# Performance work log

Measured on AMD Instinct MI355X. Metric: run time of the kernel, lower is better.

The kernel has to match this reference:

```python
import jax, jax.numpy as jnp
from jax import lax
import numpy as np

# (cin, cout, kernel, pad) for the 18 convs (funs 1,3,5,6,7,9,10,11,13..17,19..23)
CONVS = [(3,32,3,0),(32,64,3,0),(64,128,3,1),(128,64,1,0),(64,128,3,1),
         (128,256,3,1),(256,128,1,0),(128,256,3,0),(256,512,3,1),(512,256,1,0),
         (256,512,3,1),(512,256,1,0),(256,512,3,0),(512,256,3,1),(256,128,1,0),
         (128,64,3,1),(64,32,1,0),(32,6,3,1)]
# maxpool(2,2) after conv index (1-based) -> pool padding (torch pads with -inf, floor mode)
POOL_AFTER = {1: 1, 2: 1, 5: 0, 8: 1, 13: 1}
GT = (0.567, 0.469, 0.206, 0.53)  # hardcoded ground-truth box (cx, cy, w, h), normalized


def _backbone(x, ws, bs):
    for i, (w, b) in enumerate(zip(ws, bs), 1):
        pad = CONVS[i - 1][3]
        x = lax.conv_general_dilated(
            x, w, (1, 1), [(pad, pad), (pad, pad)],
            dimension_numbers=("NCHW", "OIHW", "NCHW")) + b[None, :, None, None]
        if i in POOL_AFTER:
            p = POOL_AFTER[i]
            x = lax.reduce_window(
                x, -jnp.inf, lax.max, (1, 1, 2, 2), (1, 1, 2, 2),
                [(0, 0), (0, 0), (p, p), (p, p)])
    return x


def _head(x):
    # torch: x.transpose(1,3) on [B,6,H,W] -> [B,W,H,6]; j indexes W, k indexes H
    xt = jnp.transpose(x, (0, 3, 2, 1))
    B, W, H, _ = xt.shape
    j = jnp.arange(W, dtype=xt.dtype)[None, :, None]  # [1,W,1]
    k = jnp.arange(H, dtype=xt.dtype)[None, None, :]  # [1,1,H]
    px = (j + xt[..., 2]) / W
    py = (k + xt[..., 3]) / H
    pw = jnp.exp(xt[..., 4]) / W
    ph = jnp.exp(xt[..., 5]) / H
    # center-format IoU against the single gt box (detached mask, as in torch via float())
    iw = jnp.clip(jnp.minimum(px + pw * 0.5, GT[0] + GT[2] * 0.5)
                  - jnp.maximum(px - pw * 0.5, GT[0] - GT[2] * 0.5), 0.0)
    ih = jnp.clip(jnp.minimum(py + ph * 0.5, GT[1] + GT[3] * 0.5)
                  - jnp.maximum(py - ph * 0.5, GT[1] - GT[3] * 0.5), 0.0)
    inter = iw * ih
    iou = inter / (pw * ph + GT[2] * GT[3] - inter)
    iou = lax.stop_gradient(iou)
    tx = GT[0] * W - j          # [1,W,1]
    ty = GT[1] * H - k          # [1,1,H]
    tw = np.log(GT[2] * W).astype(np.float32)
    th = np.log(GT[3] * H).astype(np.float32)
    l1 = (jnp.abs(tx - xt[..., 2]) + jnp.abs(ty - xt[..., 3])
          + jnp.abs(tw - xt[..., 4]) + jnp.abs(th - xt[..., 5]))
    loss = jnp.sum(jnp.where(iou > 0.5, l1, 0.0)).reshape(1)
    return xt, loss


def setup_inputs() -> dict:
    key = jax.random.key(0)
    keys = jax.random.split(key, 1 + 2 * len(CONVS))
    d = {"x": jax.random.normal(keys[0], (16, 3, 416, 416), jnp.float32)}
    for i, (cin, cout, ks, _) in enumerate(CONVS, 1):
        fan_in = cin * ks * ks
        d[f"w{i}"] = jax.random.normal(keys[2 * i - 1], (cout, cin, ks, ks), jnp.float32) / np.sqrt(fan_in)
        d[f"b{i}"] = jax.random.normal(keys[2 * i], (cout,), jnp.float32) * 0.01
    return d


def reference(x, w1, b1, w2, b2, w3, b3, w4, b4, w5, b5, w6, b6, w7, b7, w8, b8,
              w9, b9, w10, b10, w11, b11, w12, b12, w13, b13, w14, b14, w15, b15,
              w16, b16, w17, b17, w18, b18):
    ws = [w1, w2, w3, w4, w5, w6, w7, w8, w9, w10, w11, w12, w13, w14, w15, w16, w17, w18]
    bs = [b1, b2, b3, b4, b5, b6, b7, b8, b9, b10, b11, b12, b13, b14, b15, b16, b17, b18]
    feat = _backbone(x, ws, bs)
    xt, loss = _head(feat)
    return (xt, loss)
```

## Files before the change

kernel.cpp:

```cpp
#include <hip/hip_runtime.h>
#include <math.h>

typedef short v8s __attribute__((ext_vector_type(8)));
typedef float v4f __attribute__((ext_vector_type(4)));

template<int K, int COT, bool POOL, bool MASK, bool SWAP>
__global__ __launch_bounds__(256) void conv_fused(
    const float* __restrict__ in, const float* __restrict__ wgt,
    const float* __restrict__ bias, float* __restrict__ out,
    int B, int Cin, int Hin, int Win,
    int Hc, int Wc, int Hout, int Wout,
    int Cout, int cpad, int ppad,
    int inPS, int inRS, int inOfs, int outPS, int outRS, int outOfs)
{
    constexpr int NPY = POOL ? 2 : 1;
    constexpr int PS  = K + NPY - 1;
    const int spatial = Hout * Wout;
    const int idx = (SWAP ? blockIdx.y : blockIdx.x) * blockDim.x + threadIdx.x;
    const int cog = SWAP ? blockIdx.x : blockIdx.y;
    const int total = B * spatial;
    if (idx >= total) return;
    const int b  = idx / spatial;
    const int sp = idx - b * spatial;
    const int oy = sp / Wout;
    const int ox = sp - oy * Wout;
    const int co0 = cog * COT;

    const int cy0 = POOL ? (2 * oy - ppad) : oy;
    const int cx0 = POOL ? (2 * ox - ppad) : ox;
    const int iy0 = cy0 - cpad;
    const int ix0 = cx0 - cpad;

    bool my[PS], mx[PS];
#pragma unroll
    for (int i = 0; i < PS; i++) {
        my[i] = !MASK || ((unsigned)(iy0 + i) < (unsigned)Hin);
        mx[i] = !MASK || ((unsigned)(ix0 + i) < (unsigned)Win);
    }

    float acc[COT][NPY * NPY];
#pragma unroll
    for (int c = 0; c < COT; c++)
#pragma unroll
        for (int p = 0; p < NPY * NPY; p++) acc[c][p] = 0.f;

    const float* inB = in + inOfs + (size_t)b * Cin * inPS;
    const long wBase  = (long)co0 * Cin * K * K;

    for (int ci = 0; ci < Cin; ci++) {
        const float* ip = inB + (size_t)ci * inPS;
        float patch[PS][PS];
#pragma unroll
        for (int py = 0; py < PS; py++) {
#pragma unroll
            for (int px = 0; px < PS; px++) {
                float v = 0.f;
                if (my[py] && mx[px]) v = ip[(iy0 + py) * inRS + (ix0 + px)];
                patch[py][px] = v;
            }
        }
        const float* wp = wgt + wBase + (long)ci * K * K;
#pragma unroll
        for (int c = 0; c < COT; c++) {
#pragma unroll
            for (int kh = 0; kh < K; kh++)
#pragma unroll
            for (int kw = 0; kw < K; kw++) {
                const float wv = wp[(long)c * Cin * K * K + kh * K + kw];
#pragma unroll
                for (int dy = 0; dy < NPY; dy++)
#pragma unroll
                for (int dx = 0; dx < NPY; dx++)
                    acc[c][dy * NPY + dx] = fmaf(wv, patch[dy + kh][dx + kw],
                                                 acc[c][dy * NPY + dx]);
            }
        }
    }

#pragma unroll
    for (int c = 0; c < COT; c++) {
        float v;
        if (POOL) {
            v = -INFINITY;
#pragma unroll
            for (int dy = 0; dy < NPY; dy++)
#pragma unroll
            for (int dx = 0; dx < NPY; dx++) {
                const int cy = cy0 + dy, cx = cx0 + dx;
                if ((unsigned)cy < (unsigned)Hc && (unsigned)cx < (unsigned)Wc)
                    v = fmaxf(v, acc[c][dy * NPY + dx]);
            }
        } else {
            v = acc[c][0];
        }
        v += bias[co0 + c];
        out[outOfs + (size_t)(b * Cout + co0 + c) * outPS + oy * outRS + ox] = v;
    }
}

__global__ __launch_bounds__(256) void ring_zero(
    float* __restrict__ buf, int planes, int H, int W)
{
    int Wp = W + 2, Hp = H + 2;
    int ringlen = 2 * Wp + 2 * H;
    int t = blockIdx.x * 256 + threadIdx.x;
    if (t >= planes * ringlen) return;
    int p = t / ringlen, r = t - p * ringlen;
    float* pl = buf + (size_t)p * Hp * Wp;
    int idx;
    if (r < Wp) idx = r;
    else if (r < 2 * Wp) idx = (Hp - 1) * Wp + (r - Wp);
    else { int rr = r - 2 * Wp; int row = 1 + (rr >> 1); idx = row * Wp + ((rr & 1) ? (Wp - 1) : 0); }
    pl[idx] = 0.f;
}

__device__ __forceinline__ unsigned short f2bf_rne(float x) {
    unsigned u = __float_as_uint(x);
    return (unsigned short)((u + 0x7fffu + ((u >> 16) & 1u)) >> 16);
}
__device__ __forceinline__ float bf2f(unsigned short h) {
    return __uint_as_float(((unsigned)h) << 16);
}

__global__ __launch_bounds__(256) void prepack(
    const float* __restrict__ w, unsigned short* __restrict__ hi,
    unsigned short* __restrict__ lo, int cout, int kdim, int nkb)
{
    int t = blockIdx.x * 256 + threadIdx.x;
    if (t >= cout * kdim) return;
    int co = t / kdim, k = t - co * kdim;
    int cb = co >> 4, m = co & 15, kb = k >> 5, kk = k & 31;
    int lane = ((kk >> 3) << 4) | m, j = kk & 7;
    long dst = ((long)(cb * nkb + kb) << 9) + lane * 8 + j;
    float x = w[t];
    unsigned short h = f2bf_rne(x);
    hi[dst] = h;
    lo[dst] = f2bf_rne(x - bf2f(h));
}

template<int MT, int KS, bool SPLIT, bool DEEP>
__global__ __launch_bounds__(256) void conv_mfma(
    const float* __restrict__ in, const unsigned short* __restrict__ whi,
    const unsigned short* __restrict__ wlo, const float* __restrict__ bias,
    float* __restrict__ out, int Cin, int inHWp, int inWp, int Hc, int Wc,
    int Cout, int pad, int b0, int nb, int nkbTot, int nkbPer, int Mpad,
    int outHWp, int outWp)
{
    const int HW = Hc * Wc;
    const int M = nb * HW;
    const int tid = threadIdx.x;
    const int lane = tid & 63;
    const int wv = tid >> 6;
    const int spBase = blockIdx.x * 64;
    const int kb0 = SPLIT ? blockIdx.z * nkbPer : 0;
    const int kb1 = SPLIT ? kb0 + nkbPer : nkbTot;
    const int n = kb1 - kb0;

    __shared__ unsigned short P[DEEP ? 3 : 2][5120];

    const int spo = lane >> 2;
    const int kp  = (tid & 3) + 4 * wv;

    int jbase[4];
#pragma unroll
    for (int j = 0; j < 4; ++j) {
        int sp = spBase + spo + 16 * j;
        int q = sp < M ? sp : M - 1;
        int b = q / HW; int r = q - b * HW;
        int soy = r / Wc, sox = r - soy * Wc;
        jbase[j] = (b0 + b) * Cin * inHWp + (soy + 1) * inWp + (sox + 1);
    }

    int ci[2], r9[2], koff[2];
#pragma unroll
    for (int m = 0; m < 2; ++m) {
        int k = kb0 * 32 + 2 * kp + m;
        if (KS == 3) {
            ci[m] = k / 9; r9[m] = k - 9 * ci[m];
            int d3 = (r9[m] >= 3) + (r9[m] >= 6);
            koff[m] = ci[m] * inHWp + (d3 - pad) * inWp + (r9[m] - 3 * d3 - pad);
        } else { ci[m] = k; koff[m] = k * inHWp; }
    }

#define STAGE(RV)                                                              \
    {                                                                          \
        _Pragma("unroll")                                                      \
        for (int m = 0; m < 2; ++m)                                            \
        _Pragma("unroll")                                                      \
        for (int j = 0; j < 4; ++j)                                            \
            RV[m * 4 + j] = in[jbase[j] + koff[m]];                            \
    }
#define ADV()                                                                  \
    {                                                                          \
        _Pragma("unroll")                                                      \
        for (int m = 0; m < 2; ++m) {                                          \
            if (KS == 3) {                                                     \
                r9[m] += 5; int c_ = r9[m] >= 9; r9[m] -= c_ ? 9 : 0;          \
                ci[m] += 3 + c_;                                               \
                int d3 = (r9[m] >= 3) + (r9[m] >= 6);                          \
                koff[m] = ci[m] * inHWp + (d3 - pad) * inWp                    \
                        + (r9[m] - 3 * d3 - pad);                              \
            } else { koff[m] += 32 * inHWp; }                                  \
        }                                                                      \
    }
#define LDSW(PL, RV)                                                           \
    {                                                                          \
        _Pragma("unroll")                                                      \
        for (int j = 0; j < 4; ++j) {                                          \
            unsigned vb0 = __float_as_uint(RV[j]);                             \
            unsigned vb1 = __float_as_uint(RV[4 + j]);                         \
            unsigned hiP = (vb0 >> 16) | (vb1 & 0xffff0000u);                  \
            float r0 = RV[j]     - __uint_as_float(vb0 & 0xffff0000u);         \
            float r1 = RV[4 + j] - __uint_as_float(vb1 & 0xffff0000u);         \
            unsigned loP = (__float_as_uint(r0) >> 16)                         \
                         | (__float_as_uint(r1) & 0xffff0000u);                \
            int a = (spo + 16 * j) * 40 + 2 * kp;                              \
            *(unsigned*)((PL) + a) = hiP;                                      \
            *(unsigned*)((PL) + 2560 + a) = loP;                               \
        }                                                                      \
    }
#define MFMAPH(PL, WH, WL)                                                     \
    {                                                                          \
        _Pragma("unroll")                                                      \
        for (int nt = 0; nt < 4; ++nt) {                                       \
            int ro = (nt * 16 + (lane & 15)) * 40 + (lane >> 4) * 8;           \
            v8s ph = *(const v8s*)((PL) + ro);                                 \
            v8s pl = *(const v8s*)((PL) + 2560 + ro);                          \
            _Pragma("unroll")                                                  \
            for (int mt = 0; mt < MT; ++mt) {                                  \
                acc[mt][nt] = __builtin_amdgcn_mfma_f32_16x16x32_bf16(         \
                    WH[mt], ph, acc[mt][nt], 0, 0, 0);                         \
                acc[mt][nt] = __builtin_amdgcn_mfma_f32_16x16x32_bf16(         \
                    WH[mt], pl, acc[mt][nt], 0, 0, 0);                         \
                acc[mt][nt] = __builtin_amdgcn_mfma_f32_16x16x32_bf16(         \
                    WL[mt], ph, acc[mt][nt], 0, 0, 0);                         \
            }                                                                  \
        }                                                                      \
    }
#define WLOADTO(WH, WL)                                                        \
    {                                                                          \
        _Pragma("unroll")                                                      \
        for (int mt = 0; mt < MT; ++mt) {                                      \
            WH[mt] = *(const v8s*)whp[mt]; whp[mt] += 512;                     \
            WL[mt] = *(const v8s*)wlp[mt]; wlp[mt] += 512;                     \
        }                                                                      \
    }

    const int g0 = blockIdx.y * (MT * 4) + wv * MT;
    const unsigned short* whp[MT];
    const unsigned short* wlp[MT];
#pragma unroll
    for (int mt = 0; mt < MT; ++mt) {
        size_t base = (((size_t)(g0 + mt) * nkbTot + kb0) << 9) + lane * 8;
        whp[mt] = whi + base; wlp[mt] = wlo + base;
    }

    v4f acc[MT][4];
    {
        v4f z = {0.f, 0.f, 0.f, 0.f};
#pragma unroll
        for (int mt = 0; mt < MT; ++mt)
#pragma unroll
            for (int nt = 0; nt < 4; ++nt) acc[mt][nt] = z;
    }

    if (DEEP) {
        float rv0[8], rv1[8];
        STAGE(rv0); ADV();
        if (n > 1) { STAGE(rv1); ADV(); }
        LDSW(&P[0][0], rv0);
        if (n > 2) { STAGE(rv0); ADV(); }
        v8s whA[MT], wlA[MT], whB[MT], wlB[MT];
        WLOADTO(whA, wlA);
        __syncthreads();
        int br = 0, bw = 1;
#define ITER(C, WC, LC, WN, LN, RVX)                                           \
        {                                                                      \
            unsigned short* Pw = &P[bw][0];                                    \
            if ((C) + 1 < n) LDSW(Pw, RVX);                                    \
            if ((C) + 3 < n) { STAGE(RVX); ADV(); }                            \
            if ((C) + 1 < n) { WLOADTO(WN, LN); }                              \
            __syncthreads();                                                   \
            unsigned short* Pr = &P[br][0];                                    \
            MFMAPH(Pr, WC, LC);                                                \
            br = bw; bw = (bw == 2) ? 0 : bw + 1;                              \
        }
        int c = 0;
        for (;;) {
            ITER(c, whA, wlA, whB, wlB, rv1);
            if (++c >= n) break;
            ITER(c, whB, wlB, whA, wlA, rv0);
            if (++c >= n) break;
        }
#undef ITER
    } else {
        float rv[8];
        STAGE(rv);
        for (int cc = 0; cc < n; ++cc) {
            unsigned short* Pl = &P[cc & 1][0];
            LDSW(Pl, rv);
            __syncthreads();
            v8s wh[MT], wl[MT];
            WLOADTO(wh, wl);
            if (cc + 1 < n) { ADV(); STAGE(rv); }
            MFMAPH(Pl, wh, wl);
        }
    }
#undef STAGE
#undef ADV
#undef LDSW
#undef MFMAPH
#undef WLOADTO

    const int qrow = (lane >> 4) * 4;
    if (SPLIT) {
        float* pz = out + (size_t)blockIdx.z * Cout * Mpad;
#pragma unroll
        for (int mt = 0; mt < MT; ++mt) {
            int co = (g0 + mt) * 16 + qrow;
#pragma unroll
            for (int nt = 0; nt < 4; ++nt) {
                int sp = spBase + nt * 16 + (lane & 15);
                if (sp < M) {
#pragma unroll
                    for (int r = 0; r < 4; ++r)
                        pz[(size_t)(co + r) * Mpad + sp] = acc[mt][nt][r];
                }
            }
        }
    } else {
#pragma unroll
        for (int mt = 0; mt < MT; ++mt) {
            int co = (g0 + mt) * 16 + qrow;
            float bsv[4];
#pragma unroll
            for (int r = 0; r < 4; ++r) bsv[r] = bias[co + r];
#pragma unroll
            for (int nt = 0; nt < 4; ++nt) {
                int sp = spBase + nt * 16 + (lane & 15);
                if (sp < M) {
                    int b = sp / HW, rsp = sp - b * HW;
                    int y = rsp / Wc, xx = rsp - y * Wc;
                    float* op = out + (size_t)(b * Cout + co) * outHWp
                              + (size_t)(y + 1) * outWp + (xx + 1);
#pragma unroll
                    for (int r = 0; r < 4; ++r)
                        op[(size_t)r * outHWp] = acc[mt][nt][r] + bsv[r];
                }
            }
        }
    }
}

__global__ __launch_bounds__(256) void sk_reduce(
    const float* __restrict__ part, const float* __restrict__ bias,
    float* __restrict__ out, int Cout, int HW, int Wc, int M, int Mpad, int SK,
    int outHWp, int outWp)
{
    int t = blockIdx.x * 256 + threadIdx.x;
    if (t >= Cout * M) return;
    int co = t / M, m = t - co * M;
    float s = bias[co];
    for (int k = 0; k < SK; ++k)
        s += part[((size_t)k * Cout + co) * Mpad + m];
    int b = m / HW, rsp = m - b * HW;
    int y = rsp / Wc, xx = rsp - y * Wc;
    out[(size_t)(b * Cout + co) * outHWp + (size_t)(y + 1) * outWp + (xx + 1)] = s;
}

__global__ __launch_bounds__(256) void maxpool_k(
    const float* __restrict__ in, float* __restrict__ out,
    int Hc, int Wc, int Hp, int Wp, int p, int total,
    int inHWp, int inWp, int outHWp, int outWp)
{
    int t = blockIdx.x * 256 + threadIdx.x;
    if (t >= total) return;
    int wp2 = Hp * Wp;
    int bc = t / wp2; int r = t - bc * wp2;
    int y = r / Wp, xx = r - y * Wp;
    int y0 = 2 * y - p, x0 = 2 * xx - p;
    const float* ip = in + (size_t)bc * inHWp;
    float v = -INFINITY;
#pragma unroll
    for (int dy = 0; dy < 2; ++dy)
#pragma unroll
    for (int dx = 0; dx < 2; ++dx) {
        int yy = y0 + dy, xc = x0 + dx;
        if ((unsigned)yy < (unsigned)Hc && (unsigned)xc < (unsigned)Wc)
            v = fmaxf(v, ip[(yy + 1) * inWp + (xc + 1)]);
    }
    out[(size_t)bc * outHWp + (size_t)(y + 1) * outWp + (xx + 1)] = v;
}

__global__ __launch_bounds__(1024) void head_kernel(
    const float* __restrict__ x, float* __restrict__ out, int B)
{
    const int W = 13, H = 13;
    const float gx = 0.567f, gy = 0.469f, gw = 0.206f, gh = 0.53f;
    const int tid = threadIdx.x;
    const int total = B * W * H;
    float lsum = 0.f;
    for (int i = tid; i < total; i += blockDim.x) {
        const int b = i / (W * H);
        const int r = i - b * W * H;
        const int j = r / H;
        const int k = r - j * H;
        float v[6];
#pragma unroll
        for (int c = 0; c < 6; c++) {
            v[c] = x[((b * 6 + c) * H + k) * W + j];
            out[((b * W + j) * H + k) * 6 + c] = v[c];
        }
        const float px = (j + v[2]) / (float)W;
        const float py = (k + v[3]) / (float)H;
        const float pw = expf(v[4]) / (float)W;
        const float ph = expf(v[5]) / (float)H;
        float iw = fminf(px + pw * 0.5f, gx + gw * 0.5f)
                 - fmaxf(px - pw * 0.5f, gx - gw * 0.5f);
        iw = fmaxf(iw, 0.f);
        float ih = fminf(py + ph * 0.5f, gy + gh * 0.5f)
                 - fmaxf(py - ph * 0.5f, gy - gh * 0.5f);
        ih = fmaxf(ih, 0.f);
        const float inter = iw * ih;
        const float iou = inter / (pw * ph + gw * gh - inter);
        const float tx = gx * W - (float)j;
        const float ty = gy * H - (float)k;
        const float tw = logf(gw * W);
        const float th = logf(gh * H);
        const float l1 = fabsf(tx - v[2]) + fabsf(ty - v[3])
                       + fabsf(tw - v[4]) + fabsf(th - v[5]);
        if (iou > 0.5f) lsum += l1;
    }
    __shared__ float red[1024];
    red[tid] = lsum;
    __syncthreads();
    for (int s = blockDim.x / 2; s > 0; s >>= 1) {
        if (tid < s) red[tid] += red[tid + s];
        __syncthreads();
    }
    if (tid == 0) out[total * 6] = red[0];
}

extern "C" void kernel_launch(void* const* d_in, const int* in_sizes, int n_in,
                              void* d_out, int out_size, void* d_ws, size_t ws_size,
                              hipStream_t stream)
{
    (void)in_sizes; (void)n_in; (void)out_size;
    const float* x = (const float*)d_in[0];
    const int B = 16;
    const size_t MB = 1024 * 1024;
    char* ws = (char*)d_ws;
    float* bufA = (float*)ws;
    float* bufB = (float*)(ws + 93 * MB);
    unsigned short* WHI = (unsigned short*)(ws + 141 * MB);
    unsigned short* WLO = (unsigned short*)(ws + 153 * MB);
    char* TEMP = ws + 165 * MB;
    const bool gemmOK = ws_size >= 166 * MB;
    const size_t tempAvail = ws_size > 165 * MB ? ws_size - 165 * MB : 0;

    static const struct { int cin, cout, ks, cpad, pool, ppad; } L[18] = {
        {3,  32, 3, 0, 1, 1}, {32, 64, 3, 0, 1, 1}, {64, 128, 3, 1, 0, 0},
        {128, 64, 1, 0, 0, 0}, {64, 128, 3, 1, 1, 0}, {128, 256, 3, 1, 0, 0},
        {256, 128, 1, 0, 0, 0}, {128, 256, 3, 0, 1, 1}, {256, 512, 3, 1, 0, 0},
        {512, 256, 1, 0, 0, 0}, {256, 512, 3, 1, 0, 0}, {512, 256, 1, 0, 0, 0},
        {256, 512, 3, 0, 1, 1}, {512, 256, 3, 1, 0, 0}, {256, 128, 1, 0, 0, 0},
        {128, 64, 3, 1, 0, 0}, {64, 32, 1, 0, 0, 0}, {32, 6, 3, 1, 0, 0}
    };
    static const bool RING[18] = {0,1,0,1,1,0,0,1,0,1,0,0,1,0,1,0,1,0};

    if (gemmOK) {
        size_t off = 0;
        for (int i = 1; i <= 15; ++i) {
            int kdim = L[i].cin * L[i].ks * L[i].ks;
            int n = L[i].cout * kdim;
            prepack<<<(n + 255) / 256, 256, 0, stream>>>(
                (const float*)d_in[2 * i + 1], WHI + off, WLO + off,
                L[i].cout, kdim, kdim / 32);
            off += (size_t)n;
        }
    }

    const float* cur = x;
    int Hin = 416, Win = 416;
    size_t woff = 0;

    for (int i = 0; i < 18; ++i) {
        const auto& l = L[i];
        const int Hc = Hin + 2 * l.cpad - l.ks + 1;
        const int Wc = Win + 2 * l.cpad - l.ks + 1;
        const int Hout = l.pool ? (Hc + 2 * l.ppad - 2) / 2 + 1 : Hc;
        const int Wout = l.pool ? (Wc + 2 * l.ppad - 2) / 2 + 1 : Wc;
        float* dst = (i % 2 == 0) ? bufA : bufB;
        const float* w  = (const float*)d_in[2 * i + 1];
        const float* bb = (const float*)d_in[2 * i + 2];
        const int kdim = l.cin * l.ks * l.ks;
        const int nkb = kdim / 32;

        const int inRS  = (i == 0) ? Win : (Win + 2);
        const int inPS  = (i == 0) ? Hin * Win : (Hin + 2) * (Win + 2);
        const int inOfs = (i == 0) ? 0 : (inRS + 1);
        const bool outPad = (i != 17);
        const int outRS  = outPad ? (Wout + 2) : Wout;
        const int outPS  = outPad ? (Hout + 2) * (Wout + 2) : Hout * Wout;
        const int outOfs = outPad ? (outRS + 1) : 0;
        const int tRS = Wc + 2, tPS = (Hc + 2) * (Wc + 2);

        if (RING[i]) {
            int planes = B * l.cout;
            int ringlen = 2 * (Wout + 2) + 2 * Hout;
            ring_zero<<<(planes * ringlen + 255) / 256, 256, 0, stream>>>(
                dst, planes, Hout, Wout);
        }

        int nb = 16;
        if (l.pool) {
            size_t perImg = (size_t)l.cout * tPS * 4;
            while (nb && perImg * (size_t)nb > tempAvail) nb >>= 1;
        }
        const bool useG = gemmOK && i >= 1 && i <= 15 && (!l.pool || nb >= 1);

        if (useG) {
            for (int b0 = 0; b0 < B; b0 += nb) {
                const int M = nb * Hc * Wc;
                const int gx = (M + 63) / 64;
                const int Mpad = gx * 64;
                int MTv = (l.cout >= 256) ? 4 : (l.cout >= 128 ? 2 : 1);
                int gy = l.cout / (MTv * 64);
                int SK = 1;
                if (!l.pool) {
                    while ((long)gx * gy * SK < 512 && SK < 16 &&
                           nkb % (SK * 2) == 0 &&
                           (size_t)(SK * 2) * l.cout * (size_t)Mpad * 4 <= tempAvail)
                        SK *= 2;
                }
                const bool deep = ((long)gx * gy * SK <= 700);
                const int nkbPer = nkb / SK;
                float* gout = l.pool ? (float*)TEMP : (SK > 1 ? (float*)TEMP : dst);
                const int gHWp = l.pool ? tPS : (SK > 1 ? 0 : outPS);
                const int gWp  = l.pool ? tRS : (SK > 1 ? 0 : outRS);
                dim3 gr(gx, gy, SK);
#define GL(MTC, KSC, SPL, DP)                                                  \
                conv_mfma<MTC, KSC, SPL, DP><<<gr, 256, 0, stream>>>(          \
                    cur, WHI + woff, WLO + woff, bb, gout, l.cin, inPS, inRS,  \
                    Hc, Wc, l.cout, l.cpad, b0, nb, nkb, nkbPer, Mpad,         \
                    gHWp, gWp)
#define G3(MTC, KSC)                                                           \
                do {                                                           \
                    if (SK > 1) { if (deep) GL(MTC, KSC, true, true);          \
                                  else      GL(MTC, KSC, true, false); }       \
                    else        { if (deep) GL(MTC, KSC, false, true);         \
                                  else      GL(MTC, KSC, false, false); }      \
                } while (0)
#define G4(MTC) do { if (l.ks == 3) G3(MTC, 3); else G3(MTC, 1); } while (0)
                if (MTv == 4) G4(4);
                else if (MTv == 2) G4(2);
                else G4(1);
#undef G4
#undef G3
#undef GL
                if (SK > 1) {
                    int tot = l.cout * M;
                    sk_reduce<<<(tot + 255) / 256, 256, 0, stream>>>(
                        (const float*)TEMP, bb, dst, l.cout, Hc * Wc, Wc, M,
                        Mpad, SK, outPS, outRS);
                }
                if (l.pool) {
                    int total = nb * l.cout * Hout * Wout;
                    maxpool_k<<<(total + 255) / 256, 256, 0, stream>>>(
                        (const float*)TEMP,
                        dst + (size_t)b0 * l.cout * outPS,
                        Hc, Wc, Hout, Wout, l.ppad, total, tPS, tRS, outPS, outRS);
                }
            }
        } else {
            const int spatial = Hout * Wout;
#define FL(KK, CC, PP, MM, SW)                                                 \
            conv_fused<KK, CC, PP, MM, SW><<<                                  \
                SW ? dim3(l.cout / CC, (B * spatial + 255) / 256)              \
                   : dim3((B * spatial + 255) / 256, l.cout / CC),             \
                256, 0, stream>>>(                                             \
                cur, w, bb, dst, B, l.cin, Hin, Win, Hc, Wc, Hout, Wout,       \
                l.cout, l.cpad, l.ppad, inPS, inRS, inOfs, outPS, outRS, outOfs)
            if (i == 0)                           FL(3, 8, true, true, true);
            else if (i == 16)                     FL(1, 8, false, false, false);
            else if (i == 17)                     FL(3, 6, false, false, false);
            else if (l.pool)                      FL(3, 4, true, true, false);
            else if (l.ks == 3)                   FL(3, 8, false, true, false);
            else                                  FL(1, 8, false, true, false);
#undef FL
        }

        if (i >= 1 && i <= 15) woff += (size_t)l.cout * kdim;
        cur = dst;
        Hin = Hout;
        Win = Wout;
    }

    head_kernel<<<1, 1024, 0, stream>>>(cur, (float*)d_out, B);
}
```

Measured before the change: 1.552 ms.

## Add 128-wide spatial tile MFMA conv kernel and rebalance grid sizing

Adds a new MFMA convolution kernel that covers 128 spatial positions per block instead of 64, so each weight fragment loaded from memory is reused across twice as many columns. It is used for large layers with at most 128 output channels. For the existing kernel, the launch logic now shrinks the channel tile (MT) before falling back to split-K when the grid would have too few blocks, which avoids extra partial-sum traffic. The trade-off is more accumulator registers and LDS per block in the new kernel, and a smaller per-block weight tile on the fallback path.

```diff
diff --git a/kernel.cpp b/kernel.cpp
--- a/kernel.cpp
+++ b/kernel.cpp
@@ -352,6 +352,150 @@
     }
 }
 
+template<int MT, int KS>
+__global__ __launch_bounds__(256) void conv_mfma_n128(
+    const float* __restrict__ in, const unsigned short* __restrict__ whi,
+    const unsigned short* __restrict__ wlo, const float* __restrict__ bias,
+    float* __restrict__ out, int Cin, int inHWp, int inWp, int Hc, int Wc,
+    int Cout, int pad, int b0, int nb, int nkbTot, int outHWp, int outWp)
+{
+    const int HW = Hc * Wc;
+    const int M = nb * HW;
+    const int tid = threadIdx.x;
+    const int lane = tid & 63;
+    const int wv = tid >> 6;
+    const int spBase = blockIdx.x * 128;
+
+    __shared__ unsigned short P[10240];
+
+    const int spo = lane >> 2;
+    const int kp  = (tid & 3) + 4 * wv;
+
+    int jbase[8];
+#pragma unroll
+    for (int j = 0; j < 8; ++j) {
+        int sp = spBase + spo + 16 * j;
+        int q = sp < M ? sp : M - 1;
+        int b = q / HW; int r = q - b * HW;
+        int soy = r / Wc, sox = r - soy * Wc;
+        jbase[j] = (b0 + b) * Cin * inHWp + (soy + 1) * inWp + (sox + 1);
+    }
+
+    int ci[2], r9[2], koff[2];
+#pragma unroll
+    for (int m = 0; m < 2; ++m) {
+        int k = 2 * kp + m;
+        if (KS == 3) {
+            ci[m] = k / 9; r9[m] = k - 9 * ci[m];
+            int d3 = (r9[m] >= 3) + (r9[m] >= 6);
+            koff[m] = ci[m] * inHWp + (d3 - pad) * inWp + (r9[m] - 3 * d3 - pad);
+        } else { ci[m] = k; koff[m] = k * inHWp; }
+    }
+
+    float rv[16];
+#pragma unroll
+    for (int m = 0; m < 2; ++m)
+#pragma unroll
+    for (int j = 0; j < 8; ++j)
+        rv[m * 8 + j] = in[jbase[j] + koff[m]];
+
+    const int g0 = blockIdx.y * (MT * 4) + wv * MT;
+    const unsigned short* whp[MT];
+    const unsigned short* wlp[MT];
+#pragma unroll
+    for (int mt = 0; mt < MT; ++mt) {
+        size_t base = ((size_t)(g0 + mt) * nkbTot << 9) + lane * 8;
+        whp[mt] = whi + base; wlp[mt] = wlo + base;
+    }
+
+    v4f acc[MT][8];
+    {
+        v4f z = {0.f, 0.f, 0.f, 0.f};
+#pragma unroll
+        for (int mt = 0; mt < MT; ++mt)
+#pragma unroll
+            for (int nt = 0; nt < 8; ++nt) acc[mt][nt] = z;
+    }
+
+    for (int cc = 0; cc < nkbTot; ++cc) {
+#pragma unroll
+        for (int j = 0; j < 8; ++j) {
+            unsigned vb0 = __float_as_uint(rv[j]);
+            unsigned vb1 = __float_as_uint(rv[8 + j]);
+            unsigned hiP = (vb0 >> 16) | (vb1 & 0xffff0000u);
+            float r0 = rv[j]     - __uint_as_float(vb0 & 0xffff0000u);
+            float r1 = rv[8 + j] - __uint_as_float(vb1 & 0xffff0000u);
+            unsigned loP = (__float_as_uint(r0) >> 16)
+                         | (__float_as_uint(r1) & 0xffff0000u);
+            int a = (spo + 16 * j) * 40 + 2 * kp;
+            *(unsigned*)(P + a) = hiP;
+            *(unsigned*)(P + 5120 + a) = loP;
+        }
+        __syncthreads();
+
+        v8s wh[MT], wl[MT];
+#pragma unroll
+        for (int mt = 0; mt < MT; ++mt) {
+            wh[mt] = *(const v8s*)whp[mt]; whp[mt] += 512;
+            wl[mt] = *(const v8s*)wlp[mt]; wlp[mt] += 512;
+        }
+
+        if (cc + 1 < nkbTot) {
+#pragma unroll
+            for (int m = 0; m < 2; ++m) {
+                if (KS == 3) {
+                    r9[m] += 5; int c_ = r9[m] >= 9; r9[m] -= c_ ? 9 : 0;
+                    ci[m] += 3 + c_;
+                    int d3 = (r9[m] >= 3) + (r9[m] >= 6);
+                    koff[m] = ci[m] * inHWp + (d3 - pad) * inWp
+                            + (r9[m] - 3 * d3 - pad);
+                } else { koff[m] += 32 * inHWp; }
+            }
+#pragma unroll
+            for (int m = 0; m < 2; ++m)
+#pragma unroll
+            for (int j = 0; j < 8; ++j)
+                rv[m * 8 + j] = in[jbase[j] + koff[m]];
+        }
+
+#pragma unroll
+        for (int nt = 0; nt < 8; ++nt) {
+            int ro = (nt * 16 + (lane & 15)) * 40 + (lane >> 4) * 8;
+            v8s ph = *(const v8s*)(P + ro);
+            v8s pl = *(const v8s*)(P + 5120 + ro);
+#pragma unroll
+            for (int mt = 0; mt < MT; ++mt) {
+                acc[mt][nt] = __builtin_amdgcn_mfma_f32_16x16x32_bf16(wh[mt], ph, acc[mt][nt], 0, 0, 0);
+                acc[mt][nt] = __builtin_amdgcn_mfma_f32_16x16x32_bf16(wh[mt], pl, acc[mt][nt], 0, 0, 0);
+                acc[mt][nt] = __builtin_amdgcn_mfma_f32_16x16x32_bf16(wl[mt], ph, acc[mt][nt], 0, 0, 0);
+            }
+        }
+        __syncthreads();
+    }
+
+    const int qrow = (lane >> 4) * 4;
+#pragma unroll
+    for (int mt = 0; mt < MT; ++mt) {
+        int co = (g0 + mt) * 16 + qrow;
+        float bsv[4];
+#pragma unroll
+        for (int r = 0; r < 4; ++r) bsv[r] = bias[co + r];
+#pragma unroll
+        for (int nt = 0; nt < 8; ++nt) {
+            int sp = spBase + nt * 16 + (lane & 15);
+            if (sp < M) {
+                int b = sp / HW, rsp = sp - b * HW;
+                int y = rsp / Wc, xx = rsp - y * Wc;
+                float* op = out + (size_t)(b * Cout + co) * outHWp
+                          + (size_t)(y + 1) * outWp + (xx + 1);
+#pragma unroll
+                for (int r = 0; r < 4; ++r)
+                    op[(size_t)r * outHWp] = acc[mt][nt][r] + bsv[r];
+            }
+        }
+    }
+}
+
 __global__ __launch_bounds__(256) void sk_reduce(
     const float* __restrict__ part, const float* __restrict__ bias,
     float* __restrict__ out, int Cout, int HW, int Wc, int M, int Mpad, int SK,
@@ -522,47 +666,70 @@
         if (useG) {
             for (int b0 = 0; b0 < B; b0 += nb) {
                 const int M = nb * Hc * Wc;
-                const int gx = (M + 63) / 64;
-                const int Mpad = gx * 64;
-                int MTv = (l.cout >= 256) ? 4 : (l.cout >= 128 ? 2 : 1);
-                int gy = l.cout / (MTv * 64);
-                int SK = 1;
-                if (!l.pool) {
-                    while ((long)gx * gy * SK < 512 && SK < 16 &&
-                           nkb % (SK * 2) == 0 &&
-                           (size_t)(SK * 2) * l.cout * (size_t)Mpad * 4 <= tempAvail)
-                        SK *= 2;
-                }
-                const bool deep = ((long)gx * gy * SK <= 700);
-                const int nkbPer = nkb / SK;
-                float* gout = l.pool ? (float*)TEMP : (SK > 1 ? (float*)TEMP : dst);
-                const int gHWp = l.pool ? tPS : (SK > 1 ? 0 : outPS);
-                const int gWp  = l.pool ? tRS : (SK > 1 ? 0 : outRS);
-                dim3 gr(gx, gy, SK);
+                float* poolout = l.pool ? (float*)TEMP : dst;
+                const int pHWp = l.pool ? tPS : outPS;
+                const int pWp  = l.pool ? tRS : outRS;
+                const bool n128 = (l.cout <= 128) && ((M + 127) / 128 >= 1024);
+
+                if (n128) {
+                    const int gx = (M + 127) / 128;
+                    const int MTn = (l.cout >= 128) ? 2 : 1;
+                    dim3 gr(gx, l.cout / (MTn * 64));
+#define NL(MTC, KSC)                                                           \
+                    conv_mfma_n128<MTC, KSC><<<gr, 256, 0, stream>>>(          \
+                        cur, WHI + woff, WLO + woff, bb, poolout, l.cin, inPS, \
+                        inRS, Hc, Wc, l.cout, l.cpad, b0, nb, nkb, pHWp, pWp)
+                    if (MTn == 2) { if (l.ks == 3) NL(2, 3); else NL(2, 1); }
+                    else          { if (l.ks == 3) NL(1, 3); else NL(1, 1); }
+#undef NL
+                } else {
+                    const int gx = (M + 63) / 64;
+                    const int Mpad = gx * 64;
+                    int MTv = (l.cout >= 256) ? 4 : (l.cout >= 128 ? 2 : 1);
+                    int gy = l.cout / (MTv * 64);
+                    while (MTv > 1 && (long)gx * gy < 512) {
+                        MTv >>= 1; gy = l.cout / (MTv * 64);
+                    }
+                    int SK = 1;
+                    if (!l.pool && (long)gx * gy < 512) {
+                        MTv = (l.cout >= 256) ? 4 : (l.cout >= 128 ? 2 : 1);
+                        gy = l.cout / (MTv * 64);
+                        while ((long)gx * gy * SK < 512 && SK < 16 &&
+                               nkb % (SK * 2) == 0 &&
+                               (size_t)(SK * 2) * l.cout * (size_t)Mpad * 4 <= tempAvail)
+                            SK *= 2;
+                    }
+                    const bool deep = ((long)gx * gy * SK <= 700);
+                    const int nkbPer = nkb / SK;
+                    float* gout = (SK > 1) ? (float*)TEMP : poolout;
+                    const int gHWp = (SK > 1) ? 0 : pHWp;
+                    const int gWp  = (SK > 1) ? 0 : pWp;
+                    dim3 gr(gx, gy, SK);
 #define GL(MTC, KSC, SPL, DP)                                                  \
-                conv_mfma<MTC, KSC, SPL, DP><<<gr, 256, 0, stream>>>(          \
-                    cur, WHI + woff, WLO + woff, bb, gout, l.cin, inPS, inRS,  \
-                    Hc, Wc, l.cout, l.cpad, b0, nb, nkb, nkbPer, Mpad,         \
-                    gHWp, gWp)
+                    conv_mfma<MTC, KSC, SPL, DP><<<gr, 256, 0, stream>>>(      \
+                        cur, WHI + woff, WLO + woff, bb, gout, l.cin, inPS,    \
+                        inRS, Hc, Wc, l.cout, l.cpad, b0, nb, nkb, nkbPer,     \
+                        Mpad, gHWp, gWp)
 #define G3(MTC, KSC)                                                           \
-                do {                                                           \
-                    if (SK > 1) { if (deep) GL(MTC, KSC, true, true);          \
-                                  else      GL(MTC, KSC, true, false); }       \
-                    else        { if (deep) GL(MTC, KSC, false, true);         \
-                                  else      GL(MTC, KSC, false, false); }      \
-                } while (0)
+                    do {                                                       \
+                        if (SK > 1) { if (deep) GL(MTC, KSC, true, true);      \
+                                      else      GL(MTC, KSC, true, false); }   \
+                        else        { if (deep) GL(MTC, KSC, false, true);     \
+                                      else      GL(MTC, KSC, false, false); }  \
+                    } while (0)
 #define G4(MTC) do { if (l.ks == 3) G3(MTC, 3); else G3(MTC, 1); } while (0)
-                if (MTv == 4) G4(4);
-                else if (MTv == 2) G4(2);
-                else G4(1);
+                    if (MTv == 4) G4(4);
+                    else if (MTv == 2) G4(2);
+                    else G4(1);
 #undef G4
 #undef G3
 #undef GL
-                if (SK > 1) {
-                    int tot = l.cout * M;
-                    sk_reduce<<<(tot + 255) / 256, 256, 0, stream>>>(
-                        (const float*)TEMP, bb, dst, l.cout, Hc * Wc, Wc, M,
-                        Mpad, SK, outPS, outRS);
+                    if (SK > 1) {
+                        int tot = l.cout * M;
+                        sk_reduce<<<(tot + 255) / 256, 256, 0, stream>>>(
+                            (const float*)TEMP, bb, dst, l.cout, Hc * Wc, Wc, M,
+                            Mpad, SK, outPS, outRS);
+                    }
                 }
                 if (l.pool) {
                     int total = nb * l.cout * Hout * Wout;
```

After: 1.568 ms. About the same (+1.1%).
